# Optimization experiments

Hardware: AMD Instinct MI355X
Metric: run time of the kernel (lower is better)

## Reference

```python
import jax, jax.numpy as jnp
import numpy as np

N_NODES = 2048
N_EDGES = 8192
EDGE_DIM = 10
EDGE_HIDDEN = 32
HID = 160


def nnconv(x, edge_index, edge_attr, w1, b1, w2, b2, root, bias):
    """PyG-style NNConv with aggr='mean'.
    x: [N, HID], edge_attr: [E, EDGE_DIM], edge_index: [2, E] (src, dst).
    Per-edge weight W_e = MLP(e) reshaped to [HID, HID]; message = x[src] @ W_e,
    mean-aggregated at dst, plus root transform and bias.
    """
    n = x.shape[0]
    h = jax.nn.relu(edge_attr @ w1 + b1)                     # [E, EDGE_HIDDEN]
    W = (h @ w2 + b2).reshape(-1, HID, HID)                  # [E, HID, HID]
    src, dst = edge_index[0], edge_index[1]
    msg = jnp.einsum('ei,eio->eo', x[src], W)                # [E, HID]
    summed = jax.ops.segment_sum(msg, dst, num_segments=n)   # [N, HID]
    cnt = jax.ops.segment_sum(jnp.ones((msg.shape[0],), x.dtype), dst,
                              num_segments=n)
    aggr = summed / jnp.maximum(cnt, 1.0)[:, None]           # mean; 0 for isolated
    return aggr + x @ root + bias


def setup_inputs() -> dict:
    key = jax.random.key(0)
    ks = jax.random.split(key, 16)
    s = 1.0 / np.sqrt(HID)
    se = 1.0 / np.sqrt(EDGE_DIM)
    sh = 1.0 / np.sqrt(EDGE_HIDDEN)
    inp = {
        'x': jax.random.normal(ks[0], (N_NODES, HID), jnp.float32),
        'edge_attr': jax.random.uniform(ks[1], (N_EDGES, EDGE_DIM), jnp.float32),
        # conv1 (subgraph_conv1) params
        'w1_a': jax.random.normal(ks[2], (EDGE_DIM, EDGE_HIDDEN), jnp.float32) * se,
        'b1_a': jnp.zeros((EDGE_HIDDEN,), jnp.float32),
        'w2_a': jax.random.normal(ks[3], (EDGE_HIDDEN, HID * HID), jnp.float32) * sh,
        'b2_a': jnp.zeros((HID * HID,), jnp.float32),
        'root_a': jax.random.normal(ks[4], (HID, HID), jnp.float32) * s,
        'bias_a': jnp.zeros((HID,), jnp.float32),
        # conv2 (subgraph_conv2, applied twice) params
        'w1_b': jax.random.normal(ks[5], (EDGE_DIM, EDGE_HIDDEN), jnp.float32) * se,
        'b1_b': jnp.zeros((EDGE_HIDDEN,), jnp.float32),
        'w2_b': jax.random.normal(ks[6], (EDGE_HIDDEN, HID * HID), jnp.float32) * sh,
        'b2_b': jnp.zeros((HID * HID,), jnp.float32),
        'root_b': jax.random.normal(ks[7], (HID, HID), jnp.float32) * s,
        'bias_b': jnp.zeros((HID,), jnp.float32),
        'edge_index': jax.random.randint(ks[8], (2, N_EDGES), 0, N_NODES, jnp.int64),
    }
    return inp


def reference(x, edge_attr, w1_a, b1_a, w2_a, b2_a, root_a, bias_a,
              w1_b, b1_b, w2_b, b2_b, root_b, bias_b, edge_index):
    # subgraph_conv1 -> ReLU -> subgraph_conv2 -> ReLU -> subgraph_conv2
    h = jax.nn.relu(nnconv(x, edge_index, edge_attr,
                           w1_a, b1_a, w2_a, b2_a, root_a, bias_a))
    h = jax.nn.relu(nnconv(h, edge_index, edge_attr,
                           w1_b, b1_b, w2_b, b2_b, root_b, bias_b))
    h = nnconv(h, edge_index, edge_attr,
               w1_b, b1_b, w2_b, b2_b, root_b, bias_b)
    return h
```

## Files before the change

kernel.cpp:

```cpp
#include <hip/hip_runtime.h>

#define NN 2048
#define NE 8192
#define ED 10
#define EH 32
#define HID 160
#define NCOL 5504

typedef __attribute__((ext_vector_type(8))) short short8;
typedef __attribute__((ext_vector_type(4))) float f32x4;
typedef unsigned int u32;

__device__ __forceinline__ ushort f2bf(float v) {
    u32 u = __float_as_uint(v);
    u += 0x7FFF + ((u >> 16) & 1);
    return (ushort)(u >> 16);
}
__device__ __forceinline__ float bf2f(ushort u) {
    return __uint_as_float(((u32)u) << 16);
}
__device__ __forceinline__ void gl2lds16(const ushort* g, ushort* l) {
    __builtin_amdgcn_global_load_lds(
        (const __attribute__((address_space(1))) u32*)g,
        (__attribute__((address_space(3))) u32*)l, 16, 0, 0);
}

__global__ __launch_bounds__(256) void k_prep(
        const float* __restrict__ x, ushort* __restrict__ xb,
        const float* __restrict__ ea,
        const float* __restrict__ w1a, const float* __restrict__ b1a,
        const float* __restrict__ w1b, const float* __restrict__ b1b,
        float* __restrict__ ha, float* __restrict__ hb,
        const float* __restrict__ w2a, const float* __restrict__ b2a,
        const float* __restrict__ roota,
        const float* __restrict__ w2b, const float* __restrict__ b2b,
        const float* __restrict__ rootb,
        ushort* __restrict__ BtA, ushort* __restrict__ BtB,
        const int* __restrict__ ei, int* __restrict__ doff,
        int* __restrict__ degg, float* __restrict__ dinv,
        int* __restrict__ delist) {
    __shared__ char smem[20608];
    int b = blockIdx.x, t = threadIdx.x;

    if (b < 512) {
        int set = b >> 8, rel = b & 255;
        const float* w1 = set ? w1b : w1a;
        const float* b1 = set ? b1b : b1a;
        float* h = set ? hb : ha;
        int idx = rel * 1024 + t * 4;
        int e = idx >> 5, j0 = idx & 31;
        float o4[4];
#pragma unroll
        for (int u = 0; u < 4; ++u) {
            float acc = b1[j0 + u];
#pragma unroll
            for (int i = 0; i < ED; ++i) acc += ea[e * ED + i] * w1[i * EH + j0 + u];
            o4[u] = fmaxf(acc, 0.f);
        }
        *(float4*)&h[idx] = *(const float4*)o4;
        return;
    }
    if (b < 856) {
        int rel = b - 512;
        int set = rel / 172, pb = rel - set * 172;
        float (*tile)[161] = (float(*)[161])smem;
        const float* w2 = set ? w2b : w2a;
        const float* b2 = set ? b2b : b2a;
        const float* root = set ? rootb : roota;
        ushort* Bt = set ? BtB : BtA;
        const float* src;
        int n0, zero = 0;
        if (pb < 160)      { int q = pb / 5, op = pb - q * 5; n0 = q * 160 + op * 32; src = w2 + q * 25600 + op * 32; }
        else if (pb < 165) { int ip = pb - 160; n0 = 5120 + ip * 32; src = b2 + ip * 32; }
        else if (pb < 170) { int ip = pb - 165; n0 = 5280 + ip * 32; src = root + ip * 32; }
        else               { n0 = 5440 + (pb - 170) * 32; src = b2; zero = 1; }
        int kl = t >> 5, ol = t & 31;
#pragma unroll
        for (int pass = 0; pass < 20; ++pass) {
            int k = pass * 8 + kl;
            tile[ol][k] = zero ? 0.f : src[k * HID + ol];
        }
        __syncthreads();
        int on = t >> 3, j = t & 7;
        int n = n0 + on;
#pragma unroll
        for (int i = 0; i < 20; i += 2) {
            int k = j * 20 + i;
            u32 pk = ((u32)f2bf(tile[on][k + 1]) << 16) | f2bf(tile[on][k]);
            *(u32*)&Bt[(size_t)n * HID + k] = pk;
        }
        return;
    }
    if (b < 1176) {
        int idx = (b - 856) * 1024 + t * 4;
        float4 xv = *(const float4*)&x[idx];
        ushort o4[4] = {f2bf(xv.x), f2bf(xv.y), f2bf(xv.z), f2bf(xv.w)};
        *(u32*)&xb[idx] = *(const u32*)&o4[0];
        *(u32*)&xb[idx + 2] = *(const u32*)&o4[2];
        return;
    }
    int* deg = (int*)smem;
    int* cur = deg + NN;
    int* part = cur + NN;
    for (int i = t; i < NN; i += 256) deg[i] = 0;
    __syncthreads();
    for (int e = t; e < NE; e += 256) atomicAdd(&deg[ei[NE + e]], 1);
    __syncthreads();
    int loc[8], s = 0;
#pragma unroll
    for (int i = 0; i < 8; ++i) { loc[i] = s; s += deg[t * 8 + i]; }
    part[t] = s;
    __syncthreads();
    int tot = s;
    for (int st = 1; st < 256; st <<= 1) {
        int v = (t >= st) ? part[t - st] : 0;
        __syncthreads();
        part[t] += v;
        __syncthreads();
    }
    int base = part[t] - tot;
#pragma unroll
    for (int i = 0; i < 8; ++i) {
        int d = t * 8 + i;
        doff[d] = base + loc[i];
        cur[d] = base + loc[i];
        degg[d] = deg[d];
        dinv[d] = 1.0f / fmaxf((float)deg[d], 1.0f);
    }
    __syncthreads();
    for (int e = t; e < NE; e += 256) {
        int d = ei[NE + e];
        int p = atomicAdd(&cur[d], 1);
        delist[p] = e;
    }
}

__global__ __launch_bounds__(256) void k_gemm(const ushort* __restrict__ A,
                                              const ushort* __restrict__ B,
                                              ushort* __restrict__ G) {
    __shared__ ushort sA[128 * 32], sB[128 * 32];
    int tid = threadIdx.x;
    int bn = blockIdx.x * 128, bm = blockIdx.y * 128;
    int wid = tid >> 6, lane = tid & 63;
    int wm = (wid >> 1) * 64, wn = (wid & 1) * 64;
    int lr = lane & 15, lk = lane >> 4;
    f32x4 acc[4][4];
#pragma unroll
    for (int i = 0; i < 4; ++i)
#pragma unroll
        for (int j = 0; j < 4; ++j) acc[i][j] = (f32x4){0.f, 0.f, 0.f, 0.f};

    for (int c = 0; c < 5; ++c) {
        int k0 = c * 32;
#pragma unroll
        for (int i = 0; i < 2; ++i) {
            int s = tid + i * 256;
            int r = s >> 2, go = (s & 3) * 8;
            gl2lds16(&A[(size_t)(bm + r) * HID + k0 + go], &sA[s * 8]);
            gl2lds16(&B[(size_t)(bn + r) * HID + k0 + go], &sB[s * 8]);
        }
        __syncthreads();
        short8 av[4];
#pragma unroll
        for (int mt = 0; mt < 4; ++mt)
            av[mt] = *(const short8*)&sA[(wm + mt * 16 + lr) * 32 + lk * 8];
#pragma unroll
        for (int nt = 0; nt < 4; ++nt) {
            short8 bv = *(const short8*)&sB[(wn + nt * 16 + lr) * 32 + lk * 8];
#pragma unroll
            for (int mt = 0; mt < 4; ++mt)
                acc[mt][nt] = __builtin_amdgcn_mfma_f32_16x16x32_bf16(av[mt], bv, acc[mt][nt], 0, 0, 0);
        }
        __syncthreads();
    }
#pragma unroll
    for (int mt = 0; mt < 4; ++mt)
#pragma unroll
        for (int nt = 0; nt < 4; ++nt) {
            int m0 = bm + wm + mt * 16 + lk * 4;
            int n = bn + wn + nt * 16 + lr;
#pragma unroll
            for (int r = 0; r < 4; ++r)
                G[(size_t)(m0 + r) * NCOL + n] = f2bf(acc[mt][nt][r]);
        }
}

__global__ __launch_bounds__(160) void k_aggr(const ushort* __restrict__ G,
        const float* __restrict__ h, const int* __restrict__ ei,
        const int* __restrict__ doff, const int* __restrict__ degg,
        const float* __restrict__ dinv, const int* __restrict__ delist,
        const float* __restrict__ bias, ushort* __restrict__ xn,
        float* __restrict__ out, int last) {
    __shared__ float hbuf[16 * EH];
    __shared__ int ebuf[16], sbuf[16];
    int d = blockIdx.x, t = threadIdx.x;
    int o0 = doff[d], dg = degg[d];
    float acc = 0.f;
    for (int c0 = 0; c0 < dg; c0 += 16) {
        int nc = min(16, dg - c0);
        if (t < nc) {
            int e = delist[o0 + c0 + t];
            ebuf[t] = e;
            sbuf[t] = ei[e];
        }
        __syncthreads();
        for (int i = t; i < nc * EH; i += 160)
            hbuf[i] = h[ebuf[i >> 5] * EH + (i & 31)];
        __syncthreads();
        for (int j = 0; j < nc; ++j) {
            const ushort* Gr = G + (size_t)sbuf[j] * NCOL;
            const float* hj = &hbuf[j * EH];
            float a = bf2f(Gr[5120 + t]);
#pragma unroll
            for (int q = 0; q < 32; ++q)
                a += hj[q] * bf2f(Gr[q * HID + t]);
            acc += a;
        }
        __syncthreads();
    }
    float v = acc * dinv[d] + bf2f(G[(size_t)d * NCOL + 5280 + t]) + bias[t];
    if (last) out[d * HID + t] = v;
    else      xn[d * HID + t] = f2bf(fmaxf(v, 0.f));
}

extern "C" void kernel_launch(void* const* d_in, const int* in_sizes, int n_in,
                              void* d_out, int out_size, void* d_ws, size_t ws_size,
                              hipStream_t stream) {
    const float* x     = (const float*)d_in[0];
    const float* ea    = (const float*)d_in[1];
    const float* w1a   = (const float*)d_in[2];
    const float* b1a   = (const float*)d_in[3];
    const float* w2a   = (const float*)d_in[4];
    const float* b2a   = (const float*)d_in[5];
    const float* roota = (const float*)d_in[6];
    const float* biasa = (const float*)d_in[7];
    const float* w1b   = (const float*)d_in[8];
    const float* b1b   = (const float*)d_in[9];
    const float* w2b   = (const float*)d_in[10];
    const float* b2b   = (const float*)d_in[11];
    const float* rootb = (const float*)d_in[12];
    const float* biasb = (const float*)d_in[13];
    const int*   ei    = (const int*)d_in[14];
    float* out = (float*)d_out;

    char* p = (char*)d_ws;
    ushort* G = (ushort*)p;    p += (size_t)NN * NCOL * 2;
    ushort* BtA = (ushort*)p;  p += (size_t)NCOL * HID * 2;
    ushort* BtB = (ushort*)p;  p += (size_t)NCOL * HID * 2;
    float* h_a = (float*)p;    p += (size_t)NE * EH * 4;
    float* h_b = (float*)p;    p += (size_t)NE * EH * 4;
    ushort* xb0 = (ushort*)p;  p += (size_t)NN * HID * 2;
    ushort* xn = (ushort*)p;   p += (size_t)NN * HID * 2;
    int* doff = (int*)p;       p += NN * 4;
    int* degg = (int*)p;       p += NN * 4;
    float* dinv = (float*)p;   p += NN * 4;
    int* delist = (int*)p;     p += NE * 4;

    k_prep<<<1177, 256, 0, stream>>>(x, xb0, ea, w1a, b1a, w1b, b1b, h_a, h_b,
                                     w2a, b2a, roota, w2b, b2b, rootb, BtA, BtB,
                                     ei, doff, degg, dinv, delist);

    struct Layer { const ushort *xin, *bt; const float *h, *bias; int last; };
    Layer L[3] = {
        {xb0, BtA, h_a, biasa, 0},
        {xn,  BtB, h_b, biasb, 0},
        {xn,  BtB, h_b, biasb, 1},
    };
    for (int l = 0; l < 3; ++l) {
        k_gemm<<<dim3(NCOL / 128, NN / 128), 256, 0, stream>>>(L[l].xin, L[l].bt, G);
        k_aggr<<<NN, 160, 0, stream>>>(G, L[l].h, ei, doff, degg, dinv, delist,
                                       L[l].bias, xn, out, L[l].last);
    }
}
```

Measured before the change: 196.5 us.

## Reassociate NNConv: aggregate h⊗x per node first, then one K=5440 GEMM

Each layer now builds a per-destination feature matrix T[d] = mean over incoming edges of (h_e ⊗ x_src, x_src), with x_d appended for the root term. Then a single split-K bf16 MFMA GEMM multiplies it against a reorganized weight matrix holding w2, b2 and root, and a final reduction kernel sums the split-K partials and adds the bias. Before, a 2048x5504 G matrix was materialized and then gathered per edge. The new order removes that large intermediate write and the scattered row reads. In exchange it adds a 10-way fp32 partial buffer, an extra launch per layer, and register-heavy per-node outer-product accumulation.

New measurement: 214.2 us. 1.09x slower.

```diff
diff --git a/kernel.cpp b/kernel.cpp
--- a/kernel.cpp
+++ b/kernel.cpp
@@ -5,7 +5,8 @@
 #define ED 10
 #define EH 32
 #define HID 160
-#define NCOL 5504
+#define KT 5440
+#define KS 10
 
 typedef __attribute__((ext_vector_type(8))) short short8;
 typedef __attribute__((ext_vector_type(4))) float f32x4;
@@ -35,7 +36,7 @@
         const float* __restrict__ roota,
         const float* __restrict__ w2b, const float* __restrict__ b2b,
         const float* __restrict__ rootb,
-        ushort* __restrict__ BtA, ushort* __restrict__ BtB,
+        ushort* __restrict__ WcA, ushort* __restrict__ WcB,
         const int* __restrict__ ei, int* __restrict__ doff,
         int* __restrict__ degg, float* __restrict__ dinv,
         int* __restrict__ delist) {
@@ -60,39 +61,34 @@
         *(float4*)&h[idx] = *(const float4*)o4;
         return;
     }
-    if (b < 856) {
+    if (b < 552) {
         int rel = b - 512;
-        int set = rel / 172, pb = rel - set * 172;
-        float (*tile)[161] = (float(*)[161])smem;
+        int set = rel / 20, i0 = (rel % 20) * 8;
         const float* w2 = set ? w2b : w2a;
         const float* b2 = set ? b2b : b2a;
         const float* root = set ? rootb : roota;
-        ushort* Bt = set ? BtB : BtA;
-        const float* src;
-        int n0, zero = 0;
-        if (pb < 160)      { int q = pb / 5, op = pb - q * 5; n0 = q * 160 + op * 32; src = w2 + q * 25600 + op * 32; }
-        else if (pb < 165) { int ip = pb - 160; n0 = 5120 + ip * 32; src = b2 + ip * 32; }
-        else if (pb < 170) { int ip = pb - 165; n0 = 5280 + ip * 32; src = root + ip * 32; }
-        else               { n0 = 5440 + (pb - 170) * 32; src = b2; zero = 1; }
-        int kl = t >> 5, ol = t & 31;
-#pragma unroll
-        for (int pass = 0; pass < 20; ++pass) {
-            int k = pass * 8 + kl;
-            tile[ol][k] = zero ? 0.f : src[k * HID + ol];
-        }
-        __syncthreads();
-        int on = t >> 3, j = t & 7;
-        int n = n0 + on;
-#pragma unroll
-        for (int i = 0; i < 20; i += 2) {
-            int k = j * 20 + i;
-            u32 pk = ((u32)f2bf(tile[on][k + 1]) << 16) | f2bf(tile[on][k]);
-            *(u32*)&Bt[(size_t)n * HID + k] = pk;
+        ushort* W = set ? WcB : WcA;
+        if (t < HID) {
+#pragma unroll
+            for (int di = 0; di < 8; ++di) {
+                int i = i0 + di;
+                u32 wv[17];
+#pragma unroll
+                for (int p = 0; p < 16; ++p) {
+                    float v0 = w2[(size_t)(2 * p) * 25600 + i * HID + t];
+                    float v1 = w2[(size_t)(2 * p + 1) * 25600 + i * HID + t];
+                    wv[p] = ((u32)f2bf(v1) << 16) | f2bf(v0);
+                }
+                wv[16] = ((u32)f2bf(root[i * HID + t]) << 16) | f2bf(b2[i * HID + t]);
+#pragma unroll
+                for (int p = 0; p < 17; ++p)
+                    *(u32*)&W[(size_t)t * KT + i * 34 + 2 * p] = wv[p];
+            }
         }
         return;
     }
-    if (b < 1176) {
-        int idx = (b - 856) * 1024 + t * 4;
+    if (b < 872) {
+        int idx = (b - 552) * 1024 + t * 4;
         float4 xv = *(const float4*)&x[idx];
         ushort o4[4] = {f2bf(xv.x), f2bf(xv.y), f2bf(xv.z), f2bf(xv.w)};
         *(u32*)&xb[idx] = *(const u32*)&o4[0];
@@ -135,92 +131,122 @@
     }
 }
 
-__global__ __launch_bounds__(256) void k_gemm(const ushort* __restrict__ A,
-                                              const ushort* __restrict__ B,
-                                              ushort* __restrict__ G) {
-    __shared__ ushort sA[128 * 32], sB[128 * 32];
+__global__ __launch_bounds__(160) void k_scatter(
+        const ushort* __restrict__ xb, const float* __restrict__ h,
+        const int* __restrict__ ei, const int* __restrict__ doff,
+        const int* __restrict__ degg, const float* __restrict__ dinv,
+        const int* __restrict__ delist, ushort* __restrict__ T) {
+    __shared__ float hbuf[32 * EH];
+    __shared__ int ebuf[32], sbuf[32];
+    int d = blockIdx.x, t = threadIdx.x;
+    int o0 = doff[d], dg = degg[d];
+    float acc[33];
+#pragma unroll
+    for (int q = 0; q < 33; ++q) acc[q] = 0.f;
+    for (int c0 = 0; c0 < dg; c0 += 32) {
+        int nc = min(32, dg - c0);
+        __syncthreads();
+        if (t < 32 && c0 + t < dg) {
+            int e = delist[o0 + c0 + t];
+            ebuf[t] = e;
+            sbuf[t] = ei[e];
+        }
+        __syncthreads();
+        for (int i = t; i < nc * EH; i += 160)
+            hbuf[i] = h[(size_t)ebuf[i >> 5] * EH + (i & 31)];
+        __syncthreads();
+        for (int j = 0; j < nc; ++j) {
+            float xs = bf2f(xb[(size_t)sbuf[j] * HID + t]);
+            const float* hj = &hbuf[j * EH];
+#pragma unroll
+            for (int q = 0; q < 32; ++q) acc[q] += hj[q] * xs;
+            acc[32] += xs;
+        }
+    }
+    float di = dinv[d];
+    ushort* Trow = T + (size_t)d * KT + t * 34;
+    u32 w[17];
+#pragma unroll
+    for (int p = 0; p < 16; ++p)
+        w[p] = ((u32)f2bf(acc[2 * p + 1] * di) << 16) | f2bf(acc[2 * p] * di);
+    w[16] = ((u32)xb[(size_t)d * HID + t] << 16) | f2bf(acc[32] * di);
+#pragma unroll
+    for (int p = 0; p < 17; ++p) *(u32*)&Trow[p * 2] = w[p];
+}
+
+__global__ __launch_bounds__(256) void k_out(const ushort* __restrict__ A,
+                                             const ushort* __restrict__ B,
+                                             float* __restrict__ Cp) {
+    __shared__ ushort sA[128 * 32], sB[160 * 32];
     int tid = threadIdx.x;
-    int bn = blockIdx.x * 128, bm = blockIdx.y * 128;
+    int bm = blockIdx.x * 128;
+    int ks = blockIdx.y;
+    int k0base = ks * (KT / KS);
     int wid = tid >> 6, lane = tid & 63;
-    int wm = (wid >> 1) * 64, wn = (wid & 1) * 64;
+    int wm = (wid >> 1) * 64, wn = (wid & 1) * 80;
     int lr = lane & 15, lk = lane >> 4;
-    f32x4 acc[4][4];
+    f32x4 acc[4][5];
 #pragma unroll
     for (int i = 0; i < 4; ++i)
 #pragma unroll
-        for (int j = 0; j < 4; ++j) acc[i][j] = (f32x4){0.f, 0.f, 0.f, 0.f};
-
-    for (int c = 0; c < 5; ++c) {
-        int k0 = c * 32;
+        for (int j = 0; j < 5; ++j) acc[i][j] = (f32x4){0.f, 0.f, 0.f, 0.f};
+
+    for (int c = 0; c < 17; ++c) {
+        int k0 = k0base + c * 32;
 #pragma unroll
         for (int i = 0; i < 2; ++i) {
             int s = tid + i * 256;
             int r = s >> 2, go = (s & 3) * 8;
-            gl2lds16(&A[(size_t)(bm + r) * HID + k0 + go], &sA[s * 8]);
-            gl2lds16(&B[(size_t)(bn + r) * HID + k0 + go], &sB[s * 8]);
-        }
-        __syncthreads();
-        short8 av[4];
+            gl2lds16(&A[(size_t)(bm + r) * KT + k0 + go], &sA[s * 8]);
+        }
+#pragma unroll
+        for (int i = 0; i < 2; ++i) {
+            int s = tid + i * 256;
+            int r = s >> 2, go = (s & 3) * 8;
+            gl2lds16(&B[(size_t)r * KT + k0 + go], &sB[s * 8]);
+        }
+        if (tid < 128) {
+            int s = tid + 512;
+            int r = s >> 2, go = (s & 3) * 8;
+            gl2lds16(&B[(size_t)r * KT + k0 + go], &sB[s * 8]);
+        }
+        __syncthreads();
+        short8 av[4], bv[5];
 #pragma unroll
         for (int mt = 0; mt < 4; ++mt)
             av[mt] = *(const short8*)&sA[(wm + mt * 16 + lr) * 32 + lk * 8];
 #pragma unroll
-        for (int nt = 0; nt < 4; ++nt) {
-            short8 bv = *(const short8*)&sB[(wn + nt * 16 + lr) * 32 + lk * 8];
-#pragma unroll
-            for (int mt = 0; mt < 4; ++mt)
-                acc[mt][nt] = __builtin_amdgcn_mfma_f32_16x16x32_bf16(av[mt], bv, acc[mt][nt], 0, 0, 0);
-        }
-        __syncthreads();
-    }
+        for (int nt = 0; nt < 5; ++nt)
+            bv[nt] = *(const short8*)&sB[(wn + nt * 16 + lr) * 32 + lk * 8];
+#pragma unroll
+        for (int mt = 0; mt < 4; ++mt)
+#pragma unroll
+            for (int nt = 0; nt < 5; ++nt)
+                acc[mt][nt] = __builtin_amdgcn_mfma_f32_16x16x32_bf16(av[mt], bv[nt], acc[mt][nt], 0, 0, 0);
+        __syncthreads();
+    }
+    float* Cb = Cp + (size_t)ks * NN * HID;
 #pragma unroll
     for (int mt = 0; mt < 4; ++mt)
 #pragma unroll
-        for (int nt = 0; nt < 4; ++nt) {
+        for (int nt = 0; nt < 5; ++nt) {
             int m0 = bm + wm + mt * 16 + lk * 4;
-            int n = bn + wn + nt * 16 + lr;
+            int n = wn + nt * 16 + lr;
 #pragma unroll
             for (int r = 0; r < 4; ++r)
-                G[(size_t)(m0 + r) * NCOL + n] = f2bf(acc[mt][nt][r]);
-        }
-}
-
-__global__ __launch_bounds__(160) void k_aggr(const ushort* __restrict__ G,
-        const float* __restrict__ h, const int* __restrict__ ei,
-        const int* __restrict__ doff, const int* __restrict__ degg,
-        const float* __restrict__ dinv, const int* __restrict__ delist,
+                Cb[(size_t)(m0 + r) * HID + n] = acc[mt][nt][r];
+        }
+}
+
+__global__ __launch_bounds__(160) void k_fin(const float* __restrict__ Cp,
         const float* __restrict__ bias, ushort* __restrict__ xn,
         float* __restrict__ out, int last) {
-    __shared__ float hbuf[16 * EH];
-    __shared__ int ebuf[16], sbuf[16];
     int d = blockIdx.x, t = threadIdx.x;
-    int o0 = doff[d], dg = degg[d];
-    float acc = 0.f;
-    for (int c0 = 0; c0 < dg; c0 += 16) {
-        int nc = min(16, dg - c0);
-        if (t < nc) {
-            int e = delist[o0 + c0 + t];
-            ebuf[t] = e;
-            sbuf[t] = ei[e];
-        }
-        __syncthreads();
-        for (int i = t; i < nc * EH; i += 160)
-            hbuf[i] = h[ebuf[i >> 5] * EH + (i & 31)];
-        __syncthreads();
-        for (int j = 0; j < nc; ++j) {
-            const ushort* Gr = G + (size_t)sbuf[j] * NCOL;
-            const float* hj = &hbuf[j * EH];
-            float a = bf2f(Gr[5120 + t]);
-#pragma unroll
-            for (int q = 0; q < 32; ++q)
-                a += hj[q] * bf2f(Gr[q * HID + t]);
-            acc += a;
-        }
-        __syncthreads();
-    }
-    float v = acc * dinv[d] + bf2f(G[(size_t)d * NCOL + 5280 + t]) + bias[t];
-    if (last) out[d * HID + t] = v;
-    else      xn[d * HID + t] = f2bf(fmaxf(v, 0.f));
+    float s = bias[t];
+#pragma unroll
+    for (int p = 0; p < KS; ++p) s += Cp[(size_t)p * NN * HID + d * HID + t];
+    if (last) out[d * HID + t] = s;
+    else      xn[d * HID + t] = f2bf(fmaxf(s, 0.f));
 }
 
 extern "C" void kernel_launch(void* const* d_in, const int* in_sizes, int n_in,
@@ -244,31 +270,33 @@
     float* out = (float*)d_out;
 
     char* p = (char*)d_ws;
-    ushort* G = (ushort*)p;    p += (size_t)NN * NCOL * 2;
-    ushort* BtA = (ushort*)p;  p += (size_t)NCOL * HID * 2;
-    ushort* BtB = (ushort*)p;  p += (size_t)NCOL * HID * 2;
-    float* h_a = (float*)p;    p += (size_t)NE * EH * 4;
-    float* h_b = (float*)p;    p += (size_t)NE * EH * 4;
+    ushort* T   = (ushort*)p;  p += (size_t)NN * KT * 2;
+    ushort* WcA = (ushort*)p;  p += (size_t)HID * KT * 2;
+    ushort* WcB = (ushort*)p;  p += (size_t)HID * KT * 2;
+    float* Cp   = (float*)p;   p += (size_t)KS * NN * HID * 4;
+    float* h_a  = (float*)p;   p += (size_t)NE * EH * 4;
+    float* h_b  = (float*)p;   p += (size_t)NE * EH * 4;
     ushort* xb0 = (ushort*)p;  p += (size_t)NN * HID * 2;
-    ushort* xn = (ushort*)p;   p += (size_t)NN * HID * 2;
-    int* doff = (int*)p;       p += NN * 4;
-    int* degg = (int*)p;       p += NN * 4;
+    ushort* xn  = (ushort*)p;  p += (size_t)NN * HID * 2;
+    int* doff   = (int*)p;     p += NN * 4;
+    int* degg   = (int*)p;     p += NN * 4;
     float* dinv = (float*)p;   p += NN * 4;
     int* delist = (int*)p;     p += NE * 4;
 
-    k_prep<<<1177, 256, 0, stream>>>(x, xb0, ea, w1a, b1a, w1b, b1b, h_a, h_b,
-                                     w2a, b2a, roota, w2b, b2b, rootb, BtA, BtB,
-                                     ei, doff, degg, dinv, delist);
-
-    struct Layer { const ushort *xin, *bt; const float *h, *bias; int last; };
+    k_prep<<<873, 256, 0, stream>>>(x, xb0, ea, w1a, b1a, w1b, b1b, h_a, h_b,
+                                    w2a, b2a, roota, w2b, b2b, rootb, WcA, WcB,
+                                    ei, doff, degg, dinv, delist);
+
+    struct Layer { const ushort *xin, *wc; const float *h, *bias; int last; };
     Layer L[3] = {
-        {xb0, BtA, h_a, biasa, 0},
-        {xn,  BtB, h_b, biasb, 0},
-        {xn,  BtB, h_b, biasb, 1},
+        {xb0, WcA, h_a, biasa, 0},
+        {xn,  WcB, h_b, biasb, 0},
+        {xn,  WcB, h_b, biasb, 1},
     };
     for (int l = 0; l < 3; ++l) {
-        k_gemm<<<dim3(NCOL / 128, NN / 128), 256, 0, stream>>>(L[l].xin, L[l].bt, G);
-        k_aggr<<<NN, 160, 0, stream>>>(G, L[l].h, ei, doff, degg, dinv, delist,
-                                       L[l].bias, xn, out, L[l].last);
-    }
-}
+        k_scatter<<<NN, 160, 0, stream>>>(L[l].xin, L[l].h, ei, doff, degg,
+                                          dinv, delist, T);
+        k_out<<<dim3(NN / 128, KS), 256, 0, stream>>>(T, L[l].wc, Cp);
+        k_fin<<<NN, 160, 0, stream>>>(Cp, L[l].bias, xn, out, L[l].last);
+    }
+}
```
